# Kernel optimization log

Measured on AMD Instinct MI355X. Metric: run time of the kernel, lower is better.

The kernel has to match this reference:

```python
import jax, jax.numpy as jnp
import numpy as np

D_MODEL = 2048
N_HEADS = 16
D_HEAD = D_MODEL // N_HEADS  # 128
RANK = 32


def _orthogonal(key, rows, cols, dtype=jnp.float32):
    # mimic torch orthogonal init via QR
    a = jax.random.normal(key, (max(rows, cols), min(rows, cols)), dtype=jnp.float32)
    q, r = jnp.linalg.qr(a)
    q = q * jnp.sign(jnp.diagonal(r))
    if rows < cols:
        q = q.T
    return q.astype(dtype)


def setup_inputs() -> dict:
    key = jax.random.key(0)
    ks = jax.random.split(key, 8)
    B, T = 2, 2048
    x = jax.random.normal(ks[0], (B, T, D_MODEL), dtype=jnp.float32)
    s = 1.0 / np.sqrt(D_MODEL)
    Wq = jax.random.uniform(ks[1], (D_MODEL, D_MODEL), minval=-s, maxval=s, dtype=jnp.float32)
    Wk = jax.random.uniform(ks[2], (D_MODEL, D_MODEL), minval=-s, maxval=s, dtype=jnp.float32)
    Wv = jax.random.uniform(ks[3], (D_MODEL, D_MODEL), minval=-s, maxval=s, dtype=jnp.float32)
    Wo = jax.random.uniform(ks[4], (D_MODEL, D_MODEL), minval=-s, maxval=s, dtype=jnp.float32)
    # vein projector: project d_head -> rank, reconstruct rank -> d_head (orthogonal init)
    Wdown = _orthogonal(ks[5], D_HEAD, RANK)   # [d_head, r]
    Wup = _orthogonal(ks[6], RANK, D_HEAD)     # [r, d_head]
    return {"x": x, "Wq": Wq, "Wk": Wk, "Wv": Wv, "Wo": Wo, "Wdown": Wdown, "Wup": Wup}


def reference(x, Wq, Wk, Wv, Wo, Wdown, Wup):
    B, T, D = x.shape
    H, dh, r = N_HEADS, D_HEAD, RANK
    scale = 1.0 / np.sqrt(r)

    def heads(y):  # [B,T,D] -> [B,H,T,dh]
        return y.reshape(B, T, H, dh).transpose(0, 2, 1, 3)

    q = heads(x @ Wq.T)
    k = heads(x @ Wk.T)
    v = heads(x @ Wv.T)

    # project into vein (rank) space: [B,H,T,r]
    q_r = jnp.einsum('bhtd,dr->bhtr', q, Wdown)
    k_r = jnp.einsum('bhtd,dr->bhtr', k, Wdown)
    v_r = jnp.einsum('bhtd,dr->bhtr', v, Wdown)

    scores = jnp.einsum('bhqr,bhkr->bhqk', q_r, k_r) * scale  # [B,H,T,T]
    attn = jax.nn.softmax(scores, axis=-1)
    y_r = jnp.einsum('bhqk,bhkr->bhqr', attn, v_r)            # [B,H,T,r]
    y = jnp.einsum('bhtr,rd->bhtd', y_r, Wup)                  # reconstruct [B,H,T,dh]
    y = y.transpose(0, 2, 1, 3).reshape(B, T, D)
    out = y @ Wo.T
    return out
```

## Files before the change

### kernel.cpp

```cpp
#include <hip/hip_runtime.h>
#include <cstdint>
#include <cstddef>

typedef __bf16 bf16;
typedef __attribute__((ext_vector_type(8))) __bf16 bf16x8;
typedef __attribute__((ext_vector_type(4))) __bf16 bf16x4;
typedef __attribute__((ext_vector_type(2))) __bf16 bf16x2;
typedef __attribute__((ext_vector_type(4))) float f32x4;
typedef unsigned int u32;

#define D_MODEL 2048
#define QSCALE      0.17677669529663687f
#define QSCALE_L2E  (0.17677669529663687f * 1.4426950408889634f)

__device__ inline void async_load16(const void* gp, void* lp) {
  __builtin_amdgcn_global_load_lds(
      (const __attribute__((address_space(1))) u32*)gp,
      (__attribute__((address_space(3))) u32*)lp, 16, 0, 0);
}

__device__ inline float fast_exp2(float x) {
#if __has_builtin(__builtin_amdgcn_exp2f)
  return __builtin_amdgcn_exp2f(x);
#else
  return __expf(x * 0.6931471805599453f);
#endif
}

__global__ __launch_bounds__(256) void prep_k(
    const float* __restrict__ x,  const float* __restrict__ Wq,
    const float* __restrict__ Wk, const float* __restrict__ Wv,
    const float* __restrict__ Wo, const float* __restrict__ Wdown,
    const float* __restrict__ Wup,
    bf16* __restrict__ xb, bf16* __restrict__ EffT,
    bf16* __restrict__ WoEffT) {
  __shared__ __align__(16) char smem_[40960];
  const int bid = blockIdx.x;
  const int t = threadIdx.x;

  if (bid < 4096) {
    const int i = (bid * 256 + t) * 8;
    float4 a = *(const float4*)(x + i);
    float4 b = *(const float4*)(x + i + 4);
    bf16x8 o;
    o[0] = (bf16)a.x; o[1] = (bf16)a.y; o[2] = (bf16)a.z; o[3] = (bf16)a.w;
    o[4] = (bf16)b.x; o[5] = (bf16)b.y; o[6] = (bf16)b.z; o[7] = (bf16)b.w;
    *(bf16x8*)(xb + i) = o;
    return;
  }

  if (bid < 4864) {
    float* wd = (float*)smem_;
    for (int i = t; i < 128 * 32; i += 256) wd[i] = Wdown[i];
    __syncthreads();
    const int rel = bid - 4096;
    const int mh = rel % 48;
    const int dblk = rel / 48;
    const float* W = (mh < 16) ? Wq : ((mh < 32) ? Wk : Wv);
    const int hrow = (mh & 15) * 128;
    const int d = dblk * 128 + (t & 127);
    const int rh = (t >> 7) * 16;
    float acc[16];
#pragma unroll
    for (int j = 0; j < 16; ++j) acc[j] = 0.f;
#pragma unroll 4
    for (int k = 0; k < 128; ++k) {
      float w = W[(size_t)(hrow + k) * D_MODEL + d];
      const float* wr = wd + k * 32 + rh;
#pragma unroll
      for (int j = 0; j < 16; ++j) acc[j] += w * wr[j];
    }
    bf16* outp = EffT + (size_t)(mh * 32 + rh) * D_MODEL + d;
#pragma unroll
    for (int j = 0; j < 16; ++j) outp[(size_t)j * D_MODEL] = (bf16)acc[j];
    return;
  }

  bf16* As_ = (bf16*)smem_;
  bf16* Bs_ = (bf16*)(smem_ + 32768);
  const int rel = bid - 4864;
  const int d0 = (rel & 15) * 128, h = rel >> 4;
  const int wave = t >> 6, lane = t & 63;
  const int quad = lane >> 4, lc = lane & 15;
#pragma unroll
  for (int a = 0; a < 8; ++a) {
    int cc = a * 256 + t;
    int row = cc >> 4, c = cc & 15;
    const float* src = Wo + (size_t)(d0 + row) * 2048 + h * 128 + c * 8;
    float4 f0 = ((const float4*)src)[0], f1 = ((const float4*)src)[1];
    bf16x8 v;
    v[0] = (bf16)f0.x; v[1] = (bf16)f0.y; v[2] = (bf16)f0.z; v[3] = (bf16)f0.w;
    v[4] = (bf16)f1.x; v[5] = (bf16)f1.y; v[6] = (bf16)f1.z; v[7] = (bf16)f1.w;
    *(bf16x8*)(As_ + row * 128 + ((c ^ (row & 15)) * 8)) = v;
  }
  {
    int row = t >> 3;
    int c0 = (t & 7) * 2;
    const float* src = Wup + row * 128 + c0 * 8;
    float4 f0 = ((const float4*)src)[0], f1 = ((const float4*)src)[1];
    float4 f2 = ((const float4*)src)[2], f3 = ((const float4*)src)[3];
    bf16x8 b0, b1;
    b0[0] = (bf16)f0.x; b0[1] = (bf16)f0.y; b0[2] = (bf16)f0.z; b0[3] = (bf16)f0.w;
    b0[4] = (bf16)f1.x; b0[5] = (bf16)f1.y; b0[6] = (bf16)f1.z; b0[7] = (bf16)f1.w;
    b1[0] = (bf16)f2.x; b1[1] = (bf16)f2.y; b1[2] = (bf16)f2.z; b1[3] = (bf16)f2.w;
    b1[4] = (bf16)f3.x; b1[5] = (bf16)f3.y; b1[6] = (bf16)f3.z; b1[7] = (bf16)f3.w;
    *(bf16x8*)(Bs_ + row * 128 + ((c0 ^ (row & 15)) * 8)) = b0;
    *(bf16x8*)(Bs_ + row * 128 + (((c0 + 1) ^ (row & 15)) * 8)) = b1;
  }
  __syncthreads();
  f32x4 acc[2][2] = {};
  const int wm = wave * 32;
#pragma unroll
  for (int kc = 0; kc < 4; ++kc) {
    bf16x8 af[2], bfr[2];
#pragma unroll
    for (int mi = 0; mi < 2; ++mi) {
      int m = wm + mi * 16 + lc;
      af[mi] = *(const bf16x8*)(As_ + m * 128 + (((kc * 4 + quad) ^ (m & 15)) * 8));
    }
#pragma unroll
    for (int ni = 0; ni < 2; ++ni) {
      int n = ni * 16 + lc;
      bfr[ni] = *(const bf16x8*)(Bs_ + n * 128 + (((kc * 4 + quad) ^ (n & 15)) * 8));
    }
#pragma unroll
    for (int mi = 0; mi < 2; ++mi)
#pragma unroll
      for (int ni = 0; ni < 2; ++ni)
        acc[mi][ni] = __builtin_amdgcn_mfma_f32_16x16x32_bf16(
            af[mi], bfr[ni], acc[mi][ni], 0, 0, 0);
  }
#pragma unroll
  for (int mi = 0; mi < 2; ++mi)
#pragma unroll
    for (int ni = 0; ni < 2; ++ni)
#pragma unroll
      for (int reg = 0; reg < 4; ++reg)
        WoEffT[(size_t)(d0 + wm + mi * 16 + quad * 4 + reg) * 512 + h * 32 +
               ni * 16 + lc] = (bf16)acc[mi][ni][reg];
}

template <int EPI, int BM>
__global__ __launch_bounds__(256, (BM == 64 ? 3 : 2)) void gemm_bt_k(
    const bf16* __restrict__ A, const bf16* __restrict__ Bt,
    void* __restrict__ Cv, int M, int N, int K) {
  constexpr int MI = BM / 32;
  constexpr int AR = BM / 4;
  __shared__ __align__(16) bf16 As[2][BM * 64];
  __shared__ __align__(16) bf16 Bs[2][128 * 64];
  const int t = threadIdx.x, wave = t >> 6, lane = t & 63;
  const int quad = lane >> 4, lc = lane & 15;
  const size_t m0 = (size_t)blockIdx.x * BM;
  const size_t n0 = (size_t)blockIdx.y * 128;
  const int wm = (wave >> 1) * (MI * 16), wn = (wave & 1) * 64;
  const int sr = lane >> 3, ss = lane & 7;
  const bf16* Aga[MI]; const bf16* Bga[4]; int LoffA[MI], LoffB[4];
#pragma unroll
  for (int a = 0; a < MI; ++a) {
    int row = wave * AR + a * 8 + sr;
    Aga[a] = A + (m0 + row) * (size_t)K + (ss ^ (row & 7)) * 8;
    LoffA[a] = (wave * AR + a * 8) * 64;
  }
#pragma unroll
  for (int a = 0; a < 4; ++a) {
    int row = wave * 32 + a * 8 + sr;
    Bga[a] = Bt + (n0 + row) * (size_t)K + (ss ^ (row & 7)) * 8;
    LoffB[a] = (wave * 32 + a * 8) * 64;
  }
  f32x4 acc[MI][4] = {};
  const int NIT = K >> 6;
#pragma unroll
  for (int a = 0; a < MI; ++a) async_load16(Aga[a], &As[0][LoffA[a]]);
#pragma unroll
  for (int a = 0; a < 4; ++a) async_load16(Bga[a], &Bs[0][LoffB[a]]);
  __syncthreads();
  for (int it = 0; it < NIT; ++it) {
    const int cur = it & 1;
    if (it + 1 < NIT) {
      const int k0 = (it + 1) * 64;
#pragma unroll
      for (int a = 0; a < MI; ++a) async_load16(Aga[a] + k0, &As[1 - cur][LoffA[a]]);
#pragma unroll
      for (int a = 0; a < 4; ++a) async_load16(Bga[a] + k0, &Bs[1 - cur][LoffB[a]]);
    }
    const bf16* Asb = As[cur];
    const bf16* Bsb = Bs[cur];
#pragma unroll
    for (int kc = 0; kc < 2; ++kc) {
      bf16x8 af[MI], bfr[4];
#pragma unroll
      for (int mi = 0; mi < MI; ++mi) {
        int m = wm + mi * 16 + lc;
        af[mi] = *(const bf16x8*)(Asb + m * 64 + (((kc * 4 + quad) ^ (m & 7)) * 8));
      }
#pragma unroll
      for (int ni = 0; ni < 4; ++ni) {
        int n = wn + ni * 16 + lc;
        bfr[ni] = *(const bf16x8*)(Bsb + n * 64 + (((kc * 4 + quad) ^ (n & 7)) * 8));
      }
#pragma unroll
      for (int mi = 0; mi < MI; ++mi)
#pragma unroll
        for (int ni = 0; ni < 4; ++ni)
          acc[mi][ni] = __builtin_amdgcn_mfma_f32_16x16x32_bf16(
              af[mi], bfr[ni], acc[mi][ni], 0, 0, 0);
    }
    __syncthreads();
  }

  if (EPI == 0) {
    float* C = (float*)Cv;
#pragma unroll
    for (int mi = 0; mi < MI; ++mi)
#pragma unroll
      for (int ni = 0; ni < 4; ++ni) {
        size_t row = m0 + wm + mi * 16 + quad * 4;
        size_t col = n0 + wn + ni * 16 + lc;
#pragma unroll
        for (int reg = 0; reg < 4; ++reg)
          C[(row + reg) * (size_t)N + col] = acc[mi][ni][reg];
      }
  } else {
    bf16* C = (bf16*)Cv;
#pragma unroll
    for (int mi = 0; mi < MI; ++mi)
#pragma unroll
      for (int ni = 0; ni < 4; ++ni) {
        int n = (int)n0 + wn + ni * 16 + lc;
        int mat = n >> 9, hh = (n >> 5) & 15, r = n & 31;
        float sc = (mat == 0) ? QSCALE_L2E : 1.0f;
        int trow = (int)m0 + wm + mi * 16 + quad * 4;
        int b = trow >> 11, tl = trow & 2047;
        if (mat == 2) {
          int tile = tl >> 7, kin = tl & 127;
          size_t off = ((size_t)(b * 16 + hh) * 3 + 2) * 65536 +
                       (size_t)tile * 4096 + r * 128 +
                       (((kin >> 3) ^ (r & 15)) << 3) + (kin & 7);
          bf16x4 pk;
#pragma unroll
          for (int reg = 0; reg < 4; ++reg) pk[reg] = (bf16)acc[mi][ni][reg];
          *(bf16x4*)(C + off) = pk;
        } else {
#pragma unroll
          for (int reg = 0; reg < 4; ++reg) {
            size_t off = (((size_t)(b * 16 + hh) * 3 + mat) * 2048 + tl + reg) * 32 + r;
            C[off] = (bf16)(acc[mi][ni][reg] * sc);
          }
        }
      }
  }
}

__global__ __launch_bounds__(256, 4) void attn_k(const bf16* __restrict__ QKVr,
                                                 float* __restrict__ Op,
                                                 float* __restrict__ Sums) {
  const int bh = blockIdx.x, qb = blockIdx.y, kvh = blockIdx.z;
  const size_t base = (size_t)bh * 3 * 65536;
  const bf16* Q   = QKVr + base;
  const bf16* Kr  = Q + 65536 + (size_t)kvh * 1024 * 32;
  const bf16* Vrb = Q + 131072 + (size_t)kvh * 8 * 4096;
  __shared__ __align__(16) bf16 Ks[2][128 * 32];
  __shared__ __align__(16) bf16 Vt[2][32 * 128];
  __shared__ __align__(16) bf16 Ps[4 * 32 * 32];
  const int t = threadIdx.x, wave = t >> 6, lane = t & 63;
  const int quad = lane >> 4, lc = lane & 15;
  const int qbase = qb * 128 + wave * 32;
  const bf16x8 qf0 = *(const bf16x8*)(Q + (size_t)(qbase + lc) * 32 + quad * 8);
  const bf16x8 qf1 = *(const bf16x8*)(Q + (size_t)(qbase + 16 + lc) * 32 + quad * 8);
  f32x4 o00 = {}, o01 = {}, o10 = {}, o11 = {};
  f32x4 os0 = {}, os1 = {};
  bf16x8 ones;
#pragma unroll
  for (int j = 0; j < 8; ++j) ones[j] = (bf16)1.0f;
  const int krow = wave * 16 + (lane >> 2);
  const bf16* Kg = Kr + (size_t)krow * 32 + ((lane & 3) ^ ((krow >> 1) & 3)) * 8;
  bf16* pw = Ps + wave * 32 * 32;
  const int psw = (lc & 3) ^ (lc >> 2);

  async_load16(Kg, &Ks[0][wave * 16 * 32]);
  async_load16(Kg + (size_t)64 * 32, &Ks[0][(64 + wave * 16) * 32]);
  async_load16(Vrb + (wave * 2) * 512 + lane * 8, &Vt[0][(wave * 2) * 512]);
  async_load16(Vrb + (wave * 2 + 1) * 512 + lane * 8, &Vt[0][(wave * 2 + 1) * 512]);
  __syncthreads();

  for (int it = 0; it < 8; ++it) {
    const int kt = it * 128, cur = it & 1;
    if (it < 7) {
      async_load16(Kg + (size_t)(kt + 128) * 32, &Ks[1 - cur][wave * 16 * 32]);
      async_load16(Kg + (size_t)(kt + 192) * 32, &Ks[1 - cur][(64 + wave * 16) * 32]);
      const bf16* vg = Vrb + (size_t)(it + 1) * 4096;
      async_load16(vg + (wave * 2) * 512 + lane * 8, &Vt[1 - cur][(wave * 2) * 512]);
      async_load16(vg + (wave * 2 + 1) * 512 + lane * 8, &Vt[1 - cur][(wave * 2 + 1) * 512]);
    }
    const bf16* ksb = Ks[cur];
    const bf16* vtb = Vt[cur];
#pragma unroll
    for (int qtr = 0; qtr < 4; ++qtr) {
#pragma unroll
      for (int nii = 0; nii < 2; ++nii) {
        int ni = qtr * 2 + nii;
        int n = ni * 16 + lc;
        bf16x8 kf = *(const bf16x8*)(ksb + n * 32 + ((quad ^ ((n >> 1) & 3)) * 8));
        f32x4 z = {0.f, 0.f, 0.f, 0.f};
        f32x4 s0 = __builtin_amdgcn_mfma_f32_16x16x32_bf16(kf, qf0, z, 0, 0, 0);
        f32x4 s1 = __builtin_amdgcn_mfma_f32_16x16x32_bf16(kf, qf1, z, 0, 0, 0);
        bf16x4 p0, p1;
#pragma unroll
        for (int reg = 0; reg < 4; ++reg) {
          p0[reg] = (bf16)fast_exp2(s0[reg]);
          p1[reg] = (bf16)fast_exp2(s1[reg]);
        }
        int off = (((2 * nii + (quad >> 1)) ^ psw) * 8) + (quad & 1) * 4;
        *(bf16x4*)(pw + lc * 32 + off) = p0;
        *(bf16x4*)(pw + (16 + lc) * 32 + off) = p1;
      }
      int co = (quad ^ psw) * 8;
      bf16x8 pf0 = *(const bf16x8*)(pw + lc * 32 + co);
      bf16x8 pf1 = *(const bf16x8*)(pw + (16 + lc) * 32 + co);
      int vo = ((qtr * 4 + quad) ^ lc) * 8;
      bf16x8 v0 = *(const bf16x8*)(vtb + lc * 128 + vo);
      bf16x8 v1 = *(const bf16x8*)(vtb + (16 + lc) * 128 + vo);
      o00 = __builtin_amdgcn_mfma_f32_16x16x32_bf16(pf0, v0, o00, 0, 0, 0);
      o01 = __builtin_amdgcn_mfma_f32_16x16x32_bf16(pf0, v1, o01, 0, 0, 0);
      o10 = __builtin_amdgcn_mfma_f32_16x16x32_bf16(pf1, v0, o10, 0, 0, 0);
      o11 = __builtin_amdgcn_mfma_f32_16x16x32_bf16(pf1, v1, o11, 0, 0, 0);
      os0 = __builtin_amdgcn_mfma_f32_16x16x32_bf16(pf0, ones, os0, 0, 0, 0);
      os1 = __builtin_amdgcn_mfma_f32_16x16x32_bf16(pf1, ones, os1, 0, 0, 0);
    }
    __syncthreads();
  }
  const int b = bh >> 4, h = bh & 15;
  float* op = Op + (size_t)kvh * 4096 * 512;
#pragma unroll
  for (int reg = 0; reg < 4; ++reg) {
    size_t r0 = (size_t)b * 2048 + qbase + quad * 4 + reg;
    size_t r1 = r0 + 16;
    op[r0 * 512 + h * 32 + lc]      = o00[reg];
    op[r0 * 512 + h * 32 + 16 + lc] = o01[reg];
    op[r1 * 512 + h * 32 + lc]      = o10[reg];
    op[r1 * 512 + h * 32 + 16 + lc] = o11[reg];
  }
  if (lc == 0) {
    float* sp = Sums + (size_t)kvh * 65536 + (size_t)bh * 2048 + qbase;
#pragma unroll
    for (int reg = 0; reg < 4; ++reg) {
      sp[quad * 4 + reg]      = os0[reg];
      sp[16 + quad * 4 + reg] = os1[reg];
    }
  }
}

__global__ __launch_bounds__(256) void comb_k(const float* __restrict__ Op,
                                              const float* __restrict__ Sums,
                                              bf16* __restrict__ Yr) {
  const int idx = blockIdx.x * 256 + threadIdx.x;
  const int row = idx >> 6;
  const int c8 = (idx & 63) * 8;
  const int b = row >> 11, tl = row & 2047;
  const int h = c8 >> 5;
  const size_t si = (size_t)(b * 16 + h) * 2048 + tl;
  const float inv = 1.0f / (Sums[si] + Sums[65536 + si]);
  const float4* p0 = (const float4*)(Op + (size_t)row * 512 + c8);
  const float4* p1 = (const float4*)(Op + 4096 * 512 + (size_t)row * 512 + c8);
  float4 a0 = p0[0], a1 = p0[1];
  float4 b0 = p1[0], b1 = p1[1];
  bf16x8 o;
  o[0] = (bf16)((a0.x + b0.x) * inv); o[1] = (bf16)((a0.y + b0.y) * inv);
  o[2] = (bf16)((a0.z + b0.z) * inv); o[3] = (bf16)((a0.w + b0.w) * inv);
  o[4] = (bf16)((a1.x + b1.x) * inv); o[5] = (bf16)((a1.y + b1.y) * inv);
  o[6] = (bf16)((a1.z + b1.z) * inv); o[7] = (bf16)((a1.w + b1.w) * inv);
  *(bf16x8*)(Yr + (size_t)row * 512 + c8) = o;
}

extern "C" void kernel_launch(void* const* d_in, const int* in_sizes, int n_in,
                              void* d_out, int out_size, void* d_ws, size_t ws_size,
                              hipStream_t stream) {
  const float* x     = (const float*)d_in[0];
  const float* Wq    = (const float*)d_in[1];
  const float* Wk    = (const float*)d_in[2];
  const float* Wv    = (const float*)d_in[3];
  const float* Wo    = (const float*)d_in[4];
  const float* Wdown = (const float*)d_in[5];
  const float* Wup   = (const float*)d_in[6];
  float* out = (float*)d_out;

  char* ws = (char*)d_ws;
  bf16*  EffT   = (bf16*)(ws);
  float* Sums   = (float*)(ws);
  bf16*  WoEffT = (bf16*)(ws + 6291456);
  bf16*  QKVr   = (bf16*)(ws + 8388608);
  bf16*  Yrb    = (bf16*)(ws + 20971520);
  bf16*  xb     = (bf16*)(ws + 25165824);
  float* Opart  = (float*)(ws + 25165824);

  prep_k<<<dim3(5120), dim3(256), 0, stream>>>(x, Wq, Wk, Wv, Wo, Wdown, Wup,
                                               xb, EffT, WoEffT);
  gemm_bt_k<1, 64><<<dim3(64, 12), dim3(256), 0, stream>>>(xb, EffT, QKVr,
                                                           4096, 1536, 2048);
  attn_k<<<dim3(32, 16, 2), dim3(256), 0, stream>>>(QKVr, Opart, Sums);
  comb_k<<<dim3(1024), dim3(256), 0, stream>>>(Opart, Sums, Yrb);
  gemm_bt_k<0, 128><<<dim3(32, 16), dim3(256), 0, stream>>>(Yrb, WoEffT, out,
                                                            4096, 2048, 512);
}
```

Before: 230.9 us.

## Reorder prep blocks, batch x conversion, read Wdown via scalar loads

```diff
diff --git a/kernel.cpp b/kernel.cpp
--- a/kernel.cpp
+++ b/kernel.cpp
@@ -38,37 +38,29 @@
   const int bid = blockIdx.x;
   const int t = threadIdx.x;
 
-  if (bid < 4096) {
-    const int i = (bid * 256 + t) * 8;
-    float4 a = *(const float4*)(x + i);
-    float4 b = *(const float4*)(x + i + 4);
-    bf16x8 o;
-    o[0] = (bf16)a.x; o[1] = (bf16)a.y; o[2] = (bf16)a.z; o[3] = (bf16)a.w;
-    o[4] = (bf16)b.x; o[5] = (bf16)b.y; o[6] = (bf16)b.z; o[7] = (bf16)b.w;
-    *(bf16x8*)(xb + i) = o;
-    return;
-  }
-
-  if (bid < 4864) {
-    float* wd = (float*)smem_;
-    for (int i = t; i < 128 * 32; i += 256) wd[i] = Wdown[i];
-    __syncthreads();
-    const int rel = bid - 4096;
-    const int mh = rel % 48;
-    const int dblk = rel / 48;
+  if (bid < 768) {
+    const int mh = bid % 48;
+    const int dblk = bid / 48;
     const float* W = (mh < 16) ? Wq : ((mh < 32) ? Wk : Wv);
     const int hrow = (mh & 15) * 128;
     const int d = dblk * 128 + (t & 127);
     const int rh = (t >> 7) * 16;
+    const int rhs = __builtin_amdgcn_readfirstlane(rh);
+    const float* wdn = Wdown + rhs;
     float acc[16];
 #pragma unroll
     for (int j = 0; j < 16; ++j) acc[j] = 0.f;
-#pragma unroll 4
-    for (int k = 0; k < 128; ++k) {
-      float w = W[(size_t)(hrow + k) * D_MODEL + d];
-      const float* wr = wd + k * 32 + rh;
-#pragma unroll
-      for (int j = 0; j < 16; ++j) acc[j] += w * wr[j];
+    for (int kb = 0; kb < 16; ++kb) {
+      float wv[8];
+#pragma unroll
+      for (int u = 0; u < 8; ++u)
+        wv[u] = W[(size_t)(hrow + kb * 8 + u) * D_MODEL + d];
+#pragma unroll
+      for (int u = 0; u < 8; ++u) {
+#pragma unroll
+        for (int j = 0; j < 16; ++j)
+          acc[j] += wv[u] * wdn[(kb * 8 + u) * 32 + j];
+      }
     }
     bf16* outp = EffT + (size_t)(mh * 32 + rh) * D_MODEL + d;
 #pragma unroll
@@ -76,9 +68,31 @@
     return;
   }
 
+  if (bid >= 1024) {
+    const int tid = (bid - 1024) * 256 + t;
+    float4 v[8];
+#pragma unroll
+    for (int p = 0; p < 4; ++p) {
+      const int i = (tid + p * 262144) * 8;
+      v[2 * p]     = *(const float4*)(x + i);
+      v[2 * p + 1] = *(const float4*)(x + i + 4);
+    }
+#pragma unroll
+    for (int p = 0; p < 4; ++p) {
+      const int i = (tid + p * 262144) * 8;
+      bf16x8 o;
+      o[0] = (bf16)v[2*p].x;   o[1] = (bf16)v[2*p].y;
+      o[2] = (bf16)v[2*p].z;   o[3] = (bf16)v[2*p].w;
+      o[4] = (bf16)v[2*p+1].x; o[5] = (bf16)v[2*p+1].y;
+      o[6] = (bf16)v[2*p+1].z; o[7] = (bf16)v[2*p+1].w;
+      *(bf16x8*)(xb + i) = o;
+    }
+    return;
+  }
+
   bf16* As_ = (bf16*)smem_;
   bf16* Bs_ = (bf16*)(smem_ + 32768);
-  const int rel = bid - 4864;
+  const int rel = bid - 768;
   const int d0 = (rel & 15) * 128, h = rel >> 4;
   const int wave = t >> 6, lane = t & 63;
   const int quad = lane >> 4, lc = lane & 15;
@@ -393,7 +407,7 @@
   bf16*  xb     = (bf16*)(ws + 25165824);
   float* Opart  = (float*)(ws + 25165824);
 
-  prep_k<<<dim3(5120), dim3(256), 0, stream>>>(x, Wq, Wk, Wv, Wo, Wdown, Wup,
+  prep_k<<<dim3(2048), dim3(256), 0, stream>>>(x, Wq, Wk, Wv, Wo, Wdown, Wup,
                                                xb, EffT, WoEffT);
   gemm_bt_k<1, 64><<<dim3(64, 12), dim3(256), 0, stream>>>(xb, EffT, QKVr,
                                                            4096, 1536, 2048);
```

New measurement: 224.4 us. 1.03x faster.
